# Performance work log

Measured on AMD Instinct MI355X. Metric: run time of the kernel, lower is better.

Reference implementation:

```python
import jax, jax.numpy as jnp
import numpy as np

TGT_LEN = 1024
MEM_LEN = 1024
SAME_LENGTH = True
D_MODEL = 2048
BATCH = 4


def _make_ft_real(tgt_len: int, mem_len: int, same_length: bool) -> jnp.ndarray:
    """Build the banded Fourier mixing matrix. Since the module's input x is real
    and only .real of the output is returned, Re(FT @ x) == Re(FT) @ x, so we
    precompute only the real part (this also matches the kernel-headroom note:
    the imaginary output is never used)."""
    qlen = tgt_len
    klen = tgt_len + mem_len
    flen = klen - qlen + 1
    m = np.outer(np.arange(qlen), np.arange(flen))
    ft = np.exp(2j * np.pi * m / flen) / np.sqrt(flen)  # [qlen, flen] complex
    ft = np.pad(ft, ((0, 0), (klen - flen, 0)))          # left-pad to [qlen, klen]
    for i in range(qlen):  # setup-time numpy loop over fixed qlen rows (not traced)
        ft[i] = np.roll(ft[i], -(qlen - i - 1))
    ft = np.tril(ft, klen - qlen)
    if same_length:
        ft = np.triu(ft, 0)
    return jnp.asarray(ft.real.astype(np.float32))


_FT_REAL = _make_ft_real(TGT_LEN, MEM_LEN, SAME_LENGTH)  # [tgt_len, tgt_len+mem_len]


def setup_inputs() -> dict:
    key = jax.random.key(0)
    k1, k2 = jax.random.split(key)
    klen = TGT_LEN + MEM_LEN
    x = jax.random.normal(k1, (BATCH, klen, D_MODEL), dtype=jnp.float32)
    p = jax.random.normal(k2, (BATCH, klen, D_MODEL), dtype=jnp.float32)
    return {"x": x, "p": p, "qlen": TGT_LEN, "add_position": 1}


def reference(x, p, qlen, add_position):
    # Dropout is identity in eval mode (deterministic reference).
    if add_position:
        x = x + p
    klen = x.shape[1]
    ft = _FT_REAL[-qlen:, -klen:]                    # [qlen, klen]
    scale = np.float32(1.0 / np.sqrt(klen))
    # Banded token-mixing matmul; real part only (x is real).
    out = jnp.einsum("lm,bmd->bld", ft, x) * scale   # [B, qlen, D]
    return out
```

## Files before the change

kernel.cpp:

```cpp
#include <hip/hip_runtime.h>
#include <hip/hip_bf16.h>
#include <cstdint>

#define QLEN   1024
#define KLEN   2048
#define DMODEL 2048
#define BATCH  4
#define FLEN   (KLEN - QLEN + 1)

typedef __bf16 bf16x8 __attribute__((ext_vector_type(8)));
typedef __bf16 bf16x4 __attribute__((ext_vector_type(4)));
typedef float  f32x4  __attribute__((ext_vector_type(4)));

__device__ __bf16 g_ft[(size_t)QLEN * KLEN];
__device__ __bf16 g_yt[(size_t)BATCH * DMODEL * KLEN];

typedef __attribute__((address_space(1))) void gvoid;
typedef __attribute__((address_space(3))) void svoid;

__device__ __forceinline__ void async_load16(const void* g, void* lds) {
  gvoid* gp = (gvoid*)(uintptr_t)g;
  svoid* sp = (svoid*)(uint32_t)(uintptr_t)lds;
  __builtin_amdgcn_global_load_lds(gp, sp, 16, 0, 0);
}

__global__ void gen_ft_kernel() {
  const int u  = blockIdx.x * 256 + threadIdx.x;
  const int l  = u >> 8;
  const int m0 = (u & 255) * 8;
  const int j0 = m0 - l;
  bf16x8 o = {};
  if (j0 + 7 >= 0 && j0 < FLEN) {
    const float w     = 6.283185307179586f / (float)FLEN;
    const float scale = 1.0f / sqrtf((float)FLEN * (float)KLEN);
#pragma unroll
    for (int i = 0; i < 8; ++i) {
      const int j = j0 + i;
      float v = 0.0f;
      if (j >= 0 && j < FLEN) {
        const int r = (l * j) % FLEN;
        v = cosf((float)r * w) * scale;
      }
      o[i] = (__bf16)v;
    }
  }
  *(bf16x8*)(g_ft + (size_t)u * 8) = o;
}

__global__ __launch_bounds__(256, 4) void gen_yt_kernel(const float* __restrict__ x,
                                                        const float* __restrict__ p,
                                                        const int* __restrict__ addp) {
  __shared__ float tile[64][65];
  const int b  = blockIdx.z;
  const int m0 = blockIdx.x * 64;
  const int d0 = blockIdx.y * 64;
  const int t  = threadIdx.x;
  const float addf = (*addp) ? 1.0f : 0.0f;
  const size_t base = (size_t)b * KLEN * DMODEL;

  const int rr = t >> 4;
  const int c4 = (t & 15) * 4;
  float4 xv[4], pv[4];
#pragma unroll
  for (int it = 0; it < 4; ++it) {
    const size_t off = base + (size_t)(m0 + rr + it * 16) * DMODEL + (d0 + c4);
    xv[it] = *(const float4*)(x + off);
    pv[it] = *(const float4*)(p + off);
  }
  __builtin_amdgcn_sched_barrier(0);

#pragma unroll
  for (int it = 0; it < 4; ++it) {
    const int r = rr + it * 16;
    tile[r][c4 + 0] = xv[it].x + addf * pv[it].x;
    tile[r][c4 + 1] = xv[it].y + addf * pv[it].y;
    tile[r][c4 + 2] = xv[it].z + addf * pv[it].z;
    tile[r][c4 + 3] = xv[it].w + addf * pv[it].w;
  }
  __syncthreads();

#pragma unroll
  for (int s = 0; s < 2; ++s) {
    const int u  = t + 256 * s;
    const int d  = u >> 3;
    const int mc = u & 7;
    bf16x8 o;
#pragma unroll
    for (int i = 0; i < 8; ++i) o[i] = (__bf16)tile[mc * 8 + i][d];
    *(bf16x8*)(g_yt + base + (size_t)(d0 + d) * KLEN + (m0 + mc * 8)) = o;
  }
}

#define BM 128
#define BN 128
#define BK 64

__global__ __launch_bounds__(256) void gemm_kernel(float* __restrict__ out) {
  __shared__ __align__(16) __bf16 As[BM * BK];
  __shared__ __align__(16) __bf16 Bs[BN * BK];
  const int bn = blockIdx.x, bm = blockIdx.y, b = blockIdx.z;
  const int l0 = bm * BM, d0 = bn * BN;
  const int tid  = threadIdx.x;
  const int lane = tid & 63;
  const int wave = tid >> 6;
  const int wr = wave >> 1, wc = wave & 1;
  const int col = lane & 15, quad = lane >> 4;

  f32x4 acc[4][4] = {};

  const int t0 = l0 >> 6;
  const int t1 = (l0 + BM - 1 + FLEN - 1) >> 6;
  const __bf16* ftp = g_ft;
  const __bf16* ytp = g_yt + (size_t)b * DMODEL * KLEN;

  for (int t = t0; t <= t1; ++t) {
    const int k0 = t * BK;
#pragma unroll
    for (int s = 0; s < 4; ++s) {
      const int cb  = wave * 256 + s * 64;
      const int lc  = cb + lane;
      const int row = lc >> 3;
      const int gc8 = (lc & 7) ^ (row & 7);
      async_load16(ftp + (size_t)(l0 + row) * KLEN + k0 + gc8 * 8, As + cb * 8);
    }
#pragma unroll
    for (int s = 0; s < 4; ++s) {
      const int cb  = wave * 256 + s * 64;
      const int lc  = cb + lane;
      const int row = lc >> 3;
      const int gc8 = (lc & 7) ^ (row & 7);
      async_load16(ytp + (size_t)(d0 + row) * KLEN + k0 + gc8 * 8, Bs + cb * 8);
    }
    __syncthreads();

#pragma unroll
    for (int kk = 0; kk < 2; ++kk) {
      bf16x8 af[4], bq[4];
      const int c8 = kk * 4 + quad;
#pragma unroll
      for (int ti = 0; ti < 4; ++ti) {
        const int r = wr * 64 + ti * 16 + col;
        af[ti] = *(const bf16x8*)(As + (size_t)((r << 3) + (c8 ^ (r & 7))) * 8);
      }
#pragma unroll
      for (int tj = 0; tj < 4; ++tj) {
        const int r = wc * 64 + tj * 16 + col;
        bq[tj] = *(const bf16x8*)(Bs + (size_t)((r << 3) + (c8 ^ (r & 7))) * 8);
      }
#pragma unroll
      for (int ti = 0; ti < 4; ++ti)
#pragma unroll
        for (int tj = 0; tj < 4; ++tj)
          acc[ti][tj] = __builtin_amdgcn_mfma_f32_16x16x32_bf16(af[ti], bq[tj], acc[ti][tj], 0, 0, 0);
    }
    __syncthreads();
  }

#pragma unroll
  for (int ti = 0; ti < 4; ++ti) {
    const int l = l0 + wr * 64 + ti * 16 + quad * 4;
#pragma unroll
    for (int tj = 0; tj < 4; ++tj) {
      const int d = d0 + wc * 64 + tj * 16 + col;
      float* op = out + (size_t)b * QLEN * DMODEL + (size_t)l * DMODEL + d;
#pragma unroll
      for (int r2 = 0; r2 < 4; ++r2) op[(size_t)r2 * DMODEL] = acc[ti][tj][r2];
    }
  }
}

extern "C" void kernel_launch(void* const* d_in, const int* in_sizes, int n_in,
                              void* d_out, int out_size, void* d_ws, size_t ws_size,
                              hipStream_t stream) {
  const float* x   = (const float*)d_in[0];
  const float* p   = (const float*)d_in[1];
  const int* addp  = (const int*)d_in[3];
  float* out = (float*)d_out;

  gen_ft_kernel<<<dim3((QLEN * KLEN / 8) / 256), dim3(256), 0, stream>>>();
  gen_yt_kernel<<<dim3(KLEN / 64, DMODEL / 64, BATCH), dim3(256), 0, stream>>>(x, p, addp);
  gemm_kernel<<<dim3(DMODEL / BN, QLEN / BM, BATCH), dim3(256), 0, stream>>>(out);
}
```

Before: 207.1 us.

## Pipeline transpose kernel with async global-to-LDS double buffering

The x+p transpose/convert kernel now has each block walk eight 64-row tiles. Loads go through global_load_lds into double-buffered, XOR-swizzled LDS tiles, with manual waitcnt and barriers so the next tile's loads overlap conversion of the current one. This is meant to hide global-load latency and avoid staging through registers, at the cost of fewer blocks (512 instead of 4096) and larger LDS use (64 KB per block). The hand-coded waitcnt encodings are fragile.

Result: no change. 209.9 us (+1.3%).

```diff
diff --git a/kernel.cpp b/kernel.cpp
--- a/kernel.cpp
+++ b/kernel.cpp
@@ -47,47 +47,64 @@
   *(bf16x8*)(g_ft + (size_t)u * 8) = o;
 }
 
-__global__ __launch_bounds__(256, 4) void gen_yt_kernel(const float* __restrict__ x,
-                                                        const float* __restrict__ p,
-                                                        const int* __restrict__ addp) {
-  __shared__ float tile[64][65];
-  const int b  = blockIdx.z;
-  const int m0 = blockIdx.x * 64;
-  const int d0 = blockIdx.y * 64;
-  const int t  = threadIdx.x;
+__global__ __launch_bounds__(256) void gen_yt_kernel(const float* __restrict__ x,
+                                                     const float* __restrict__ p,
+                                                     const int* __restrict__ addp) {
+  __shared__ __align__(16) float xt[2][64 * 64];
+  __shared__ __align__(16) float pt[2][64 * 64];
+  const int tid  = threadIdx.x;
+  const int lane = tid & 63;
+  const int wave = tid >> 6;
   const float addf = (*addp) ? 1.0f : 0.0f;
+  const int b      = blockIdx.z;
+  const int d0     = blockIdx.y * 64;
+  const int m_base = blockIdx.x * 512;
   const size_t base = (size_t)b * KLEN * DMODEL;
 
-  const int rr = t >> 4;
-  const int c4 = (t & 15) * 4;
-  float4 xv[4], pv[4];
-#pragma unroll
-  for (int it = 0; it < 4; ++it) {
-    const size_t off = base + (size_t)(m0 + rr + it * 16) * DMODEL + (d0 + c4);
-    xv[it] = *(const float4*)(x + off);
-    pv[it] = *(const float4*)(p + off);
-  }
-  __builtin_amdgcn_sched_barrier(0);
-
-#pragma unroll
-  for (int it = 0; it < 4; ++it) {
-    const int r = rr + it * 16;
-    tile[r][c4 + 0] = xv[it].x + addf * pv[it].x;
-    tile[r][c4 + 1] = xv[it].y + addf * pv[it].y;
-    tile[r][c4 + 2] = xv[it].z + addf * pv[it].z;
-    tile[r][c4 + 3] = xv[it].w + addf * pv[it].w;
-  }
-  __syncthreads();
-
-#pragma unroll
-  for (int s = 0; s < 2; ++s) {
-    const int u  = t + 256 * s;
-    const int d  = u >> 3;
-    const int mc = u & 7;
-    bf16x8 o;
-#pragma unroll
-    for (int i = 0; i < 8; ++i) o[i] = (__bf16)tile[mc * 8 + i][d];
-    *(bf16x8*)(g_yt + base + (size_t)(d0 + d) * KLEN + (m0 + mc * 8)) = o;
+  const int lrow = lane >> 4;
+  const int lchk = lane & 15;
+
+  auto issue = [&](int t, int bb) {
+    const int m0 = m_base + t * 64;
+#pragma unroll
+    for (int s = 0; s < 4; ++s) {
+      const int r0 = wave * 16 + s * 4;
+      const int K  = ((r0 >> 3) & 7) << 1;
+      const int gc = lchk ^ K;
+      const size_t go = base + (size_t)(m0 + r0 + lrow) * DMODEL + d0 + gc * 4;
+      async_load16(x + go, &xt[bb][r0 * 64]);
+      async_load16(p + go, &pt[bb][r0 * 64]);
+    }
+  };
+
+  auto consume = [&](int t, int bb) {
+    const int m0 = m_base + t * 64;
+#pragma unroll
+    for (int s = 0; s < 2; ++s) {
+      const int u  = tid + 256 * s;
+      const int d  = u >> 3;
+      const int mc = u & 7;
+      bf16x8 o;
+#pragma unroll
+      for (int i = 0; i < 8; ++i) {
+        const int m   = mc * 8 + i;
+        const int idx = m * 64 + ((d >> 2) ^ (mc << 1)) * 4 + (d & 3);
+        o[i] = (__bf16)(xt[bb][idx] + addf * pt[bb][idx]);
+      }
+      *(bf16x8*)(g_yt + base + (size_t)(d0 + d) * KLEN + (m0 + mc * 8)) = o;
+    }
+  };
+
+  issue(0, 0);
+#pragma unroll
+  for (int t = 0; t < 8; ++t) {
+    asm volatile("s_barrier" ::: "memory");
+    if (t < 7) issue(t + 1, (t + 1) & 1);
+    if (t == 0)      __builtin_amdgcn_s_waitcnt(0x0F78);
+    else if (t < 7)  __builtin_amdgcn_s_waitcnt(0x0F7A);
+    else             __builtin_amdgcn_s_waitcnt(0x0F72);
+    asm volatile("s_barrier" ::: "memory");
+    consume(t, t & 1);
   }
 }
 
@@ -178,6 +195,6 @@
   float* out = (float*)d_out;
 
   gen_ft_kernel<<<dim3((QLEN * KLEN / 8) / 256), dim3(256), 0, stream>>>();
-  gen_yt_kernel<<<dim3(KLEN / 64, DMODEL / 64, BATCH), dim3(256), 0, stream>>>(x, p, addp);
+  gen_yt_kernel<<<dim3(4, 32, BATCH), dim3(256), 0, stream>>>(x, p, addp);
   gemm_kernel<<<dim3(DMODEL / BN, QLEN / BM, BATCH), dim3(256), 0, stream>>>(out);
 }
```
